# Optimization experiments

Measured on AMD Instinct MI355X. Metric: run time of the kernel, lower is better.

## Reference

```python
import jax, jax.numpy as jnp
import numpy as np

N_NODES = 100000
N_EDGES = 3200000
EMBED_DIM = 64
BATCH = 16384


def setup_inputs() -> dict:
    key = jax.random.key(0)
    k1, k2, k3, k4 = jax.random.split(key, 4)
    gcn_weight = jax.random.normal(k1, (N_NODES, EMBED_DIM), dtype=jnp.float32) * 0.1
    gcn_bias = jnp.zeros((EMBED_DIM,), dtype=jnp.float32)
    linear_weight = jax.random.normal(k2, (N_NODES, 1), dtype=jnp.float32) * 0.1
    linear_bias = jnp.zeros((1,), dtype=jnp.float32)
    edge_index = jax.random.randint(k3, (2, N_EDGES), 0, N_NODES, dtype=jnp.int64)
    interaction_pairs = jax.random.randint(k4, (BATCH, 2), 0, N_NODES, dtype=jnp.int64)
    return {
        "gcn_weight": gcn_weight,
        "gcn_bias": gcn_bias,
        "linear_weight": linear_weight,
        "linear_bias": linear_bias,
        "edge_index": edge_index,
        "interaction_pairs": interaction_pairs,
    }


def _gcn_conv_identity_features(gcn_weight, gcn_bias, edge_index):
    # Features X = I, so X @ W = W. GCNConv output = D^{-1/2}(A+I)D^{-1/2} W + b.
    src, dst = edge_index[0], edge_index[1]
    ones = jnp.ones((src.shape[0],), dtype=gcn_weight.dtype)
    # degree (with self loop) computed on destination nodes, as in PyG gcn_norm
    deg = jax.ops.segment_sum(ones, dst, num_segments=N_NODES) + 1.0
    dinv = jax.lax.rsqrt(deg)  # [N]
    norm = dinv[src] * dinv[dst]  # [E]
    msg = gcn_weight[src] * norm[:, None]  # [E, D] -- dominant memory traffic
    agg = jax.ops.segment_sum(msg, dst, num_segments=N_NODES)  # [N, D]
    # self-loop term: norm_ii = 1/deg[i]
    out = agg + gcn_weight * (dinv * dinv)[:, None] + gcn_bias
    return out


def reference(gcn_weight, gcn_bias, linear_weight, linear_bias, edge_index, interaction_pairs):
    node_emb = _gcn_conv_identity_features(gcn_weight, gcn_bias, edge_index)  # [N, D]
    e = node_emb[interaction_pairs]  # [B, 2, D] gather
    # FM pairwise interaction: 0.5 * sum_d ((sum_f e)^2 - sum_f e^2)
    sum_sq = jnp.square(jnp.sum(e, axis=1))  # [B, D]
    sq_sum = jnp.sum(jnp.square(e), axis=1)  # [B, D]
    fm = 0.5 * jnp.sum(sum_sq - sq_sum, axis=1, keepdims=True)  # [B, 1]
    # FeaturesLinear: sum of per-node scalar embeddings + bias
    lin = jnp.sum(linear_weight[interaction_pairs], axis=1) + linear_bias  # [B, 1]
    return jnp.squeeze(lin + fm, axis=1)  # [B]
```

## Files before the change

kernel.cpp:

```cpp
#include <hip/hip_runtime.h>

#define N_NODES 100000
#define N_EDGES 3200000
#define BATCH 16384
#define MAX_SLOTS 32768

#define NW 12500
#define SLICES 256
#define EPS2 12500
#define I4PS2 3125

#define NBUCK 256
#define BCAP 8192
#define BCAP_SH 13
#define EBCAP 4608

#define HIST_THREADS 1024
#define HGSIZE (SLICES * HIST_THREADS)

#define OFF_SLOT      0
#define OFF_DINV      400000
#define OFF_NODELIST  800000
#define OFF_GCUR      931072
#define OFF_PARTIALS  932096
#define OFF_WH        13732096
#define OFF_BINS      26532096
#define OFF_EMB       34920704

__device__ __forceinline__ unsigned bfr(float f) {
    unsigned u = __float_as_uint(f);
    return (u + 0x7FFFu + ((u >> 16) & 1u)) >> 16;
}
__device__ __forceinline__ float bfx(unsigned h) {
    return __uint_as_float(h << 16);
}

__global__ void k_flags(const int* __restrict__ pairs, unsigned* __restrict__ slot,
                        int* __restrict__ nodelist, unsigned* __restrict__ gcur) {
    int i = blockIdx.x * blockDim.x + threadIdx.x;
    if (i < NBUCK) gcur[i] = (unsigned)(i << BCAP_SH);
    if (i < 2 * BATCH) {
        int n = pairs[i];
        nodelist[i] = n;
        slot[n] = (unsigned)(i + 1);
    }
}

__device__ __forceinline__ int cert(int d, const unsigned* __restrict__ slot,
                                    const int* __restrict__ nodelist) {
    unsigned r = slot[d];
    unsigned idx = r - 1u;
    if (idx < (unsigned)MAX_SLOTS && nodelist[idx] == d) return (int)idx;
    return -1;
}

__global__ void k_hist(const int* __restrict__ src, const int* __restrict__ dst,
                       const unsigned* __restrict__ slot, const int* __restrict__ nodelist,
                       unsigned* __restrict__ partials, unsigned* __restrict__ gcur,
                       unsigned* __restrict__ bins,
                       const float4* __restrict__ w4, uint4* __restrict__ wh4) {
    __shared__ unsigned h[NW];
    __shared__ unsigned ebuf[EBCAP];
    __shared__ int lc[NBUCK];
    __shared__ int base[NBUCK];
    __shared__ int ecnt;
    int g = blockIdx.x;
    int tid = threadIdx.x;
    int lane = tid & 63;
    for (int i = tid; i < NW; i += HIST_THREADS) h[i] = 0;
    if (tid < NBUCK) lc[tid] = 0;
    if (tid == 0) ecnt = 0;
    __syncthreads();
    const int4* d4 = (const int4*)(dst + g * EPS2);
    const int4* s4 = (const int4*)(src + g * EPS2);
    for (int i = tid; i < I4PS2; i += HIST_THREADS) {
        int4 v = d4[i];
        int4 s = s4[i];
        atomicAdd(&h[v.x >> 3], 1u << ((v.x & 7) << 2));
        atomicAdd(&h[v.y >> 3], 1u << ((v.y & 7) << 2));
        atomicAdd(&h[v.z >> 3], 1u << ((v.z & 7) << 2));
        atomicAdd(&h[v.w >> 3], 1u << ((v.w & 7) << 2));
#define STAGE(dc, sc)                                                          \
        {                                                                      \
            int t = cert(dc, slot, nodelist);                                  \
            unsigned long long mk = __ballot(t >= 0);                          \
            int bs = 0;                                                        \
            if (lane == 0) bs = atomicAdd(&ecnt, (int)__popcll(mk));           \
            bs = __shfl(bs, 0, 64);                                            \
            if (t >= 0) {                                                      \
                int off = bs + (int)__popcll(mk & ((1ull << lane) - 1ull));    \
                if (off < EBCAP) {                                             \
                    ebuf[off] = ((unsigned)t << 17) | (unsigned)(sc);          \
                    atomicAdd(&lc[t >> 7], 1);                                 \
                }                                                              \
            }                                                                  \
        }
        STAGE(v.x, s.x)
        STAGE(v.y, s.y)
        STAGE(v.z, s.z)
        STAGE(v.w, s.w)
#undef STAGE
    }
    __syncthreads();
    unsigned* outp = partials + (unsigned)g * NW;
    for (int i = tid; i < NW; i += HIST_THREADS) outp[i] = h[i];
    if (tid < NBUCK) {
        base[tid] = (int)atomicAdd(&gcur[tid], (unsigned)lc[tid]);
        lc[tid] = 0;
    }
    __syncthreads();
    int ne = ecnt;
    if (ne > EBCAP) ne = EBCAP;
    for (int j = tid; j < ne; j += HIST_THREADS) {
        unsigned e = ebuf[j];
        int b = (int)(e >> 24);
        int r = atomicAdd(&lc[b], 1);
        unsigned pos = (unsigned)base[b] + (unsigned)r;
        if (pos < (unsigned)((b + 1) << BCAP_SH)) bins[pos] = e;
    }
    for (int k = g * HIST_THREADS + tid; k < N_NODES * 8; k += HGSIZE) {
        float4 va = w4[k * 2];
        float4 vb = w4[k * 2 + 1];
        uint4 o;
        o.x = bfr(va.x) | (bfr(va.y) << 16);
        o.y = bfr(va.z) | (bfr(va.w) << 16);
        o.z = bfr(vb.x) | (bfr(vb.y) << 16);
        o.w = bfr(vb.z) | (bfr(vb.w) << 16);
        wh4[k] = o;
    }
}

__global__ void k_mid(const unsigned* __restrict__ partials, float* __restrict__ dinv) {
    __shared__ unsigned pA[256], pB[256], pC[256], pD[256];
    int blk = blockIdx.x;
    int wi = threadIdx.x & 31, sg = threadIdx.x >> 5;
    int w = blk * 32 + wi;
    unsigned A = 0, B = 0, C = 0, D = 0;
    if (w < NW) {
        const unsigned* q = partials + w;
#pragma unroll
        for (int ch = 0; ch < 2; ++ch) {
            unsigned x = 0, y = 0;
#pragma unroll
            for (int k = 0; k < 16; ++k) {
                unsigned v = q[(unsigned)(sg * 32 + ch * 16 + k) * NW];
                x += v & 0x0F0F0F0Fu;
                y += (v >> 4) & 0x0F0F0F0Fu;
            }
            A += x & 0x00FF00FFu;
            B += (x >> 8) & 0x00FF00FFu;
            C += y & 0x00FF00FFu;
            D += (y >> 8) & 0x00FF00FFu;
        }
    }
    pA[threadIdx.x] = A; pB[threadIdx.x] = B; pC[threadIdx.x] = C; pD[threadIdx.x] = D;
    __syncthreads();
    if (threadIdx.x < 32 && w < NW) {
        unsigned sA = 0, sB = 0, sC = 0, sD = 0;
#pragma unroll
        for (int k = 0; k < 8; ++k) {
            sA += pA[k * 32 + wi]; sB += pB[k * 32 + wi];
            sC += pC[k * 32 + wi]; sD += pD[k * 32 + wi];
        }
        float4 d0, d1;
        d0.x = rsqrtf((float)(sA & 0xFFFFu) + 1.0f);
        d0.y = rsqrtf((float)(sC & 0xFFFFu) + 1.0f);
        d0.z = rsqrtf((float)(sB & 0xFFFFu) + 1.0f);
        d0.w = rsqrtf((float)(sD & 0xFFFFu) + 1.0f);
        d1.x = rsqrtf((float)(sA >> 16) + 1.0f);
        d1.y = rsqrtf((float)(sC >> 16) + 1.0f);
        d1.z = rsqrtf((float)(sB >> 16) + 1.0f);
        d1.w = rsqrtf((float)(sD >> 16) + 1.0f);
        ((float4*)dinv)[w * 2] = d0;
        ((float4*)dinv)[w * 2 + 1] = d1;
    }
}

__global__ void k_gfuse(const unsigned* __restrict__ gcur, const unsigned* __restrict__ bins,
                        const int* __restrict__ nodelist, const uint4* __restrict__ wh4,
                        const float* __restrict__ dinv, const float4* __restrict__ bias4,
                        uint4* __restrict__ emb4) {
    __shared__ unsigned ebuf2[BCAP];
    __shared__ int lc[128], st[128];
    int b = blockIdx.x >> 1;
    int half = blockIdx.x & 1;
    int tid = threadIdx.x;
    int cnt = (int)(gcur[b] - (unsigned)(b << BCAP_SH));
    if (cnt > BCAP) cnt = BCAP;
    const unsigned* bp = bins + ((unsigned)b << BCAP_SH);
    if (tid < 128) lc[tid] = 0;
    __syncthreads();
    for (int j = tid; j < cnt; j += 1024) atomicAdd(&lc[(bp[j] >> 17) & 127], 1);
    __syncthreads();
    if (tid < 128) st[tid] = lc[tid];
    __syncthreads();
    for (int off = 1; off < 128; off <<= 1) {
        int v = (tid < 128 && tid >= off) ? st[tid - off] : 0;
        __syncthreads();
        if (tid < 128) st[tid] += v;
        __syncthreads();
    }
    if (tid < 128) {
        st[tid] -= lc[tid];
        lc[tid] = st[tid];
    }
    __syncthreads();
    for (int j = tid; j < cnt; j += 1024) {
        unsigned e = bp[j];
        int r = atomicAdd(&lc[(e >> 17) & 127], 1);
        ebuf2[r] = e & 0x1FFFFu;
    }
    __syncthreads();
    int wave = tid >> 6, lane = tid & 63;
    int rg = lane >> 3, dp = lane & 7;
#pragma unroll 1
    for (int q = 0; q < 4; ++q) {
        int sl = half * 64 + wave * 4 + q;
        int s0 = st[sl];
        int cn = lc[sl] - s0;
        double a0 = 0., a1 = 0., a2 = 0., a3 = 0., a4 = 0., a5 = 0., a6 = 0., a7 = 0.;
        int j = 0;
        for (; j + 16 <= cn; j += 16) {
            int e0 = (int)ebuf2[s0 + j + rg];
            int e1 = (int)ebuf2[s0 + j + 8 + rg];
            float dv0 = dinv[e0], dv1 = dinv[e1];
            uint4 oa = wh4[(e0 << 3) + dp];
            uint4 ob = wh4[(e1 << 3) + dp];
            a0 += (double)(bfx(oa.x) * dv0 + bfx(ob.x) * dv1);
            a1 += (double)(bfx(oa.x >> 16) * dv0 + bfx(ob.x >> 16) * dv1);
            a2 += (double)(bfx(oa.y) * dv0 + bfx(ob.y) * dv1);
            a3 += (double)(bfx(oa.y >> 16) * dv0 + bfx(ob.y >> 16) * dv1);
            a4 += (double)(bfx(oa.z) * dv0 + bfx(ob.z) * dv1);
            a5 += (double)(bfx(oa.z >> 16) * dv0 + bfx(ob.z >> 16) * dv1);
            a6 += (double)(bfx(oa.w) * dv0 + bfx(ob.w) * dv1);
            a7 += (double)(bfx(oa.w >> 16) * dv0 + bfx(ob.w >> 16) * dv1);
        }
        for (; j < cn; j += 8) {
            if (rg < cn - j) {
                int e0 = (int)ebuf2[s0 + j + rg];
                float dv0 = dinv[e0];
                uint4 oa = wh4[(e0 << 3) + dp];
                a0 += (double)(bfx(oa.x) * dv0);
                a1 += (double)(bfx(oa.x >> 16) * dv0);
                a2 += (double)(bfx(oa.y) * dv0);
                a3 += (double)(bfx(oa.y >> 16) * dv0);
                a4 += (double)(bfx(oa.z) * dv0);
                a5 += (double)(bfx(oa.z >> 16) * dv0);
                a6 += (double)(bfx(oa.w) * dv0);
                a7 += (double)(bfx(oa.w >> 16) * dv0);
            }
        }
#pragma unroll
        for (int m = 8; m <= 32; m <<= 1) {
            a0 += __shfl_xor(a0, m, 64); a1 += __shfl_xor(a1, m, 64);
            a2 += __shfl_xor(a2, m, 64); a3 += __shfl_xor(a3, m, 64);
            a4 += __shfl_xor(a4, m, 64); a5 += __shfl_xor(a5, m, 64);
            a6 += __shfl_xor(a6, m, 64); a7 += __shfl_xor(a7, m, 64);
        }
        if (rg == 0) {
            int gslot = (b << 7) + sl;
            int n = nodelist[gslot];
            float dn = dinv[n];
            uint4 u = wh4[(n << 3) + dp];
            float4 b0 = bias4[dp * 2], b1 = bias4[dp * 2 + 1];
            float r0 = ((float)a0 + bfx(u.x) * dn) * dn + b0.x;
            float r1 = ((float)a1 + bfx(u.x >> 16) * dn) * dn + b0.y;
            float r2 = ((float)a2 + bfx(u.y) * dn) * dn + b0.z;
            float r3 = ((float)a3 + bfx(u.y >> 16) * dn) * dn + b0.w;
            float r4 = ((float)a4 + bfx(u.z) * dn) * dn + b1.x;
            float r5 = ((float)a5 + bfx(u.z >> 16) * dn) * dn + b1.y;
            float r6 = ((float)a6 + bfx(u.w) * dn) * dn + b1.z;
            float r7 = ((float)a7 + bfx(u.w >> 16) * dn) * dn + b1.w;
            uint4 o;
            o.x = bfr(r0) | (bfr(r1) << 16);
            o.y = bfr(r2) | (bfr(r3) << 16);
            o.z = bfr(r4) | (bfr(r5) << 16);
            o.w = bfr(r6) | (bfr(r7) << 16);
            emb4[(gslot << 3) + dp] = o;
        }
    }
}

__global__ void k_final(const int* __restrict__ pairs, const unsigned* __restrict__ slot,
                        const uint2* __restrict__ emb2, const float* __restrict__ lw,
                        const float* __restrict__ lb, float* __restrict__ out) {
    int p = (blockIdx.x * blockDim.x + threadIdx.x) >> 4;
    int li = threadIdx.x & 15;
    if (p >= BATCH) return;
    int a = pairs[p * 2], b = pairs[p * 2 + 1];
    int sa = (int)slot[a] - 1;
    int sb = (int)slot[b] - 1;
    uint2 ua = emb2[(sa << 4) + li];
    uint2 ub = emb2[(sb << 4) + li];
    float prod = bfx(ua.x) * bfx(ub.x) + bfx(ua.x >> 16) * bfx(ub.x >> 16)
               + bfx(ua.y) * bfx(ub.y) + bfx(ua.y >> 16) * bfx(ub.y >> 16);
#pragma unroll
    for (int m = 1; m <= 8; m <<= 1) prod += __shfl_xor(prod, m, 64);
    if (li == 0) out[p] = lw[a] + lw[b] + lb[0] + prod;
}

extern "C" void kernel_launch(void* const* d_in, const int* in_sizes, int n_in,
                              void* d_out, int out_size, void* d_ws, size_t ws_size,
                              hipStream_t stream) {
    const float* gcn_weight    = (const float*)d_in[0];
    const float* gcn_bias      = (const float*)d_in[1];
    const float* linear_weight = (const float*)d_in[2];
    const float* linear_bias   = (const float*)d_in[3];
    const int*   edge_index    = (const int*)d_in[4];
    const int*   pairs         = (const int*)d_in[5];
    float* out = (float*)d_out;

    char* ws = (char*)d_ws;
    unsigned* slot      = (unsigned*)(ws + OFF_SLOT);
    float*    dinv      = (float*)   (ws + OFF_DINV);
    int*      nodelist  = (int*)     (ws + OFF_NODELIST);
    unsigned* gcur      = (unsigned*)(ws + OFF_GCUR);
    unsigned* partials  = (unsigned*)(ws + OFF_PARTIALS);
    uint4*    wh4       = (uint4*)   (ws + OFF_WH);
    unsigned* bins      = (unsigned*)(ws + OFF_BINS);
    uint4*    emb4      = (uint4*)   (ws + OFF_EMB);
    uint2*    emb2      = (uint2*)   (ws + OFF_EMB);

    const int* src_arr = edge_index;
    const int* dst_arr = edge_index + N_EDGES;

    k_flags<<<64, 512, 0, stream>>>(pairs, slot, nodelist, gcur);
    k_hist<<<SLICES, HIST_THREADS, 0, stream>>>(src_arr, dst_arr, slot, nodelist,
                                                partials, gcur, bins,
                                                (const float4*)gcn_weight, wh4);
    k_mid<<<391, 256, 0, stream>>>(partials, dinv);
    k_gfuse<<<NBUCK * 2, 1024, 0, stream>>>(gcur, bins, nodelist, wh4,
                                            dinv, (const float4*)gcn_bias, emb4);
    k_final<<<1024, 256, 0, stream>>>(pairs, slot, emb2, linear_weight, linear_bias, out);
}
```

Baseline: 158.7 us.

## Halve bucket size so each gfuse block sorts only its own 64 slots

Bucket count goes from 256 to 512 and per-bucket capacity from 8192 to 4096 entries. Each k_gfuse block now owns one bucket of 64 slots instead of two blocks redundantly counting and scattering the same 128-slot bucket. The aim is to remove the duplicated bin-reading and local sorting work. The histogram zeroing, partial write-out and ebuf flush in k_hist are also vectorized to uint4. The risk is overflow of the smaller bucket capacity, where excess entries are dropped.

```diff
diff --git a/kernel.cpp b/kernel.cpp
--- a/kernel.cpp
+++ b/kernel.cpp
@@ -6,14 +6,16 @@
 #define MAX_SLOTS 32768
 
 #define NW 12500
+#define NW4 3125
 #define SLICES 256
 #define EPS2 12500
 #define I4PS2 3125
 
-#define NBUCK 256
-#define BCAP 8192
-#define BCAP_SH 13
+#define NBUCK 512
+#define BCAP 4096
+#define BCAP_SH 12
 #define EBCAP 4608
+#define EBCAP4 1152
 
 #define HIST_THREADS 1024
 #define HGSIZE (SLICES * HIST_THREADS)
@@ -22,10 +24,10 @@
 #define OFF_DINV      400000
 #define OFF_NODELIST  800000
 #define OFF_GCUR      931072
-#define OFF_PARTIALS  932096
-#define OFF_WH        13732096
-#define OFF_BINS      26532096
-#define OFF_EMB       34920704
+#define OFF_PARTIALS  933120
+#define OFF_WH        13733120
+#define OFF_BINS      26533120
+#define OFF_EMB       34921728
 
 __device__ __forceinline__ unsigned bfr(float f) {
     unsigned u = __float_as_uint(f);
@@ -67,7 +69,8 @@
     int g = blockIdx.x;
     int tid = threadIdx.x;
     int lane = tid & 63;
-    for (int i = tid; i < NW; i += HIST_THREADS) h[i] = 0;
+    uint4* h4 = (uint4*)h;
+    for (int i = tid; i < NW4; i += HIST_THREADS) h4[i] = make_uint4(0u, 0u, 0u, 0u);
     if (tid < NBUCK) lc[tid] = 0;
     if (tid == 0) ecnt = 0;
     __syncthreads();
@@ -91,7 +94,7 @@
                 int off = bs + (int)__popcll(mk & ((1ull << lane) - 1ull));    \
                 if (off < EBCAP) {                                             \
                     ebuf[off] = ((unsigned)t << 17) | (unsigned)(sc);          \
-                    atomicAdd(&lc[t >> 7], 1);                                 \
+                    atomicAdd(&lc[t >> 6], 1);                                 \
                 }                                                              \
             }                                                                  \
         }
@@ -102,8 +105,8 @@
 #undef STAGE
     }
     __syncthreads();
-    unsigned* outp = partials + (unsigned)g * NW;
-    for (int i = tid; i < NW; i += HIST_THREADS) outp[i] = h[i];
+    uint4* outp4 = (uint4*)(partials + (unsigned)g * NW);
+    for (int i = tid; i < NW4; i += HIST_THREADS) outp4[i] = h4[i];
     if (tid < NBUCK) {
         base[tid] = (int)atomicAdd(&gcur[tid], (unsigned)lc[tid]);
         lc[tid] = 0;
@@ -111,12 +114,22 @@
     __syncthreads();
     int ne = ecnt;
     if (ne > EBCAP) ne = EBCAP;
-    for (int j = tid; j < ne; j += HIST_THREADS) {
-        unsigned e = ebuf[j];
-        int b = (int)(e >> 24);
-        int r = atomicAdd(&lc[b], 1);
-        unsigned pos = (unsigned)base[b] + (unsigned)r;
-        if (pos < (unsigned)((b + 1) << BCAP_SH)) bins[pos] = e;
+    const uint4* ebuf4 = (const uint4*)ebuf;
+    for (int j4 = tid; j4 * 4 < ne; j4 += HIST_THREADS) {
+        uint4 e4 = ebuf4[j4];
+#define FLUSH(ee, kk)                                                          \
+        if (j4 * 4 + kk < ne) {                                                \
+            unsigned e = (ee);                                                 \
+            int b = (int)(e >> 23);                               \
+            int r = atomicAdd(&lc[b], 1);                                      \
+            unsigned pos = (unsigned)base[b] + (unsigned)r;                    \
+            if (pos < (unsigned)((b + 1) << BCAP_SH)) bins[pos] = e;           \
+        }
+        FLUSH(e4.x, 0)
+        FLUSH(e4.y, 1)
+        FLUSH(e4.z, 2)
+        FLUSH(e4.w, 3)
+#undef FLUSH
     }
     for (int k = g * HIST_THREADS + tid; k < N_NODES * 8; k += HGSIZE) {
         float4 va = w4[k * 2];
@@ -181,33 +194,32 @@
                         const float* __restrict__ dinv, const float4* __restrict__ bias4,
                         uint4* __restrict__ emb4) {
     __shared__ unsigned ebuf2[BCAP];
-    __shared__ int lc[128], st[128];
-    int b = blockIdx.x >> 1;
-    int half = blockIdx.x & 1;
+    __shared__ int lc[64], st[64];
+    int b = blockIdx.x;
     int tid = threadIdx.x;
     int cnt = (int)(gcur[b] - (unsigned)(b << BCAP_SH));
     if (cnt > BCAP) cnt = BCAP;
     const unsigned* bp = bins + ((unsigned)b << BCAP_SH);
-    if (tid < 128) lc[tid] = 0;
-    __syncthreads();
-    for (int j = tid; j < cnt; j += 1024) atomicAdd(&lc[(bp[j] >> 17) & 127], 1);
-    __syncthreads();
-    if (tid < 128) st[tid] = lc[tid];
-    __syncthreads();
-    for (int off = 1; off < 128; off <<= 1) {
-        int v = (tid < 128 && tid >= off) ? st[tid - off] : 0;
+    if (tid < 64) lc[tid] = 0;
+    __syncthreads();
+    for (int j = tid; j < cnt; j += 1024) atomicAdd(&lc[(bp[j] >> 17) & 63], 1);
+    __syncthreads();
+    if (tid < 64) st[tid] = lc[tid];
+    __syncthreads();
+    for (int off = 1; off < 64; off <<= 1) {
+        int v = (tid < 64 && tid >= off) ? st[tid - off] : 0;
         __syncthreads();
-        if (tid < 128) st[tid] += v;
+        if (tid < 64) st[tid] += v;
         __syncthreads();
     }
-    if (tid < 128) {
+    if (tid < 64) {
         st[tid] -= lc[tid];
         lc[tid] = st[tid];
     }
     __syncthreads();
     for (int j = tid; j < cnt; j += 1024) {
         unsigned e = bp[j];
-        int r = atomicAdd(&lc[(e >> 17) & 127], 1);
+        int r = atomicAdd(&lc[(e >> 17) & 63], 1);
         ebuf2[r] = e & 0x1FFFFu;
     }
     __syncthreads();
@@ -215,7 +227,7 @@
     int rg = lane >> 3, dp = lane & 7;
 #pragma unroll 1
     for (int q = 0; q < 4; ++q) {
-        int sl = half * 64 + wave * 4 + q;
+        int sl = wave * 4 + q;
         int s0 = st[sl];
         int cn = lc[sl] - s0;
         double a0 = 0., a1 = 0., a2 = 0., a3 = 0., a4 = 0., a5 = 0., a6 = 0., a7 = 0.;
@@ -258,7 +270,7 @@
             a6 += __shfl_xor(a6, m, 64); a7 += __shfl_xor(a7, m, 64);
         }
         if (rg == 0) {
-            int gslot = (b << 7) + sl;
+            int gslot = (b << 6) + sl;
             int n = nodelist[gslot];
             float dn = dinv[n];
             uint4 u = wh4[(n << 3) + dp];
@@ -329,7 +341,7 @@
                                                 partials, gcur, bins,
                                                 (const float4*)gcn_weight, wh4);
     k_mid<<<391, 256, 0, stream>>>(partials, dinv);
-    k_gfuse<<<NBUCK * 2, 1024, 0, stream>>>(gcur, bins, nodelist, wh4,
-                                            dinv, (const float4*)gcn_bias, emb4);
+    k_gfuse<<<NBUCK, 1024, 0, stream>>>(gcur, bins, nodelist, wh4,
+                                        dinv, (const float4*)gcn_bias, emb4);
     k_final<<<1024, 256, 0, stream>>>(pairs, slot, emb2, linear_weight, linear_bias, out);
 }
```

Measured after the change: 161.5 us. About the same (+1.8%).
